# Performance work log

Hardware: AMD Instinct MI355X
Metric: run time of the kernel (lower is better)

The kernel has to match this reference:

```python
import jax, jax.numpy as jnp
import numpy as np

B, H, W, C = 16, 32, 32, 512
HEADS, DHEAD = 8, 64  # head * channel == C
GROUPS, EPS = 32, 1e-5


def setup_inputs() -> dict:
    key = jax.random.key(0)
    ks = jax.random.split(key, 6)
    return {
        "x": jax.random.normal(ks[0], (B, H, W, C), jnp.float32),
        "gn_gamma": jnp.ones((C,), jnp.float32),
        "gn_beta": jnp.zeros((C,), jnp.float32),
        "wq": jax.random.normal(ks[1], (C, HEADS * DHEAD), jnp.float32) * 0.02,
        "wk": jax.random.normal(ks[2], (C, HEADS * DHEAD), jnp.float32) * 0.02,
        "wv": jax.random.normal(ks[3], (C, HEADS * DHEAD), jnp.float32) * 0.02,
        "conv_w": jax.random.normal(ks[4], (3, 3, HEADS * DHEAD, C), jnp.float32) * 0.02,
        "conv_b": jnp.zeros((C,), jnp.float32),
    }


def _group_norm(x, gamma, beta):
    b, h, w, c = x.shape
    xg = x.reshape(b, h, w, GROUPS, c // GROUPS)
    mean = jnp.mean(xg, axis=(1, 2, 4), keepdims=True)
    var = jnp.var(xg, axis=(1, 2, 4), keepdims=True)
    xn = (xg - mean) * jax.lax.rsqrt(var + EPS)
    return xn.reshape(b, h, w, c) * gamma + beta


def reference(x, gn_gamma, gn_beta, wq, wk, wv, conv_w, conv_b):
    xn = _group_norm(x, gn_gamma, gn_beta)          # [B,H,W,C]
    t = xn.reshape(B, H * W, C)                      # tokens [B,S,C]
    q = (t @ wq).reshape(B, H * W, HEADS, DHEAD)
    k = (t @ wk).reshape(B, H * W, HEADS, DHEAD)
    v = (t @ wv).reshape(B, H * W, HEADS, DHEAD)
    scale = 1.0 / jnp.sqrt(jnp.asarray(DHEAD, q.dtype))
    scores = jnp.einsum("bqhd,bkhd->bhqk", q, k) * scale  # [B,HEADS,S,S]
    weights = jax.nn.softmax(scores, axis=-1)
    out = jnp.einsum("bhqk,bkhd->bqhd", weights, v)       # [B,S,HEADS,DHEAD]
    out = out.reshape(B, H, W, HEADS * DHEAD)
    y = jax.lax.conv_general_dilated(
        out, conv_w, window_strides=(1, 1), padding=((1, 1), (1, 1)),
        dimension_numbers=("NHWC", "HWIO", "NHWC")) + conv_b
    return y + x
```

## Files before the change

kernel.cpp:

```cpp
#include <hip/hip_runtime.h>
#include <hip/hip_bf16.h>

#define Bn 16
#define Cc 512
#define Ss 1024
#define HEADS 8
#define DHEAD 64
#define GROUPS 32
#define CPG 16
#define EPSv 1e-5f
#define Mtok (Bn*Ss)
#define QKVS 1536
#define PROW 34
#define PIMG (PROW*PROW)

typedef __hip_bfloat16 bf16;
typedef __attribute__((ext_vector_type(8))) short short8;
typedef __attribute__((ext_vector_type(4))) float f32x4;

union U4 { uint4 u; bf16 h[8]; };
union B4 { ushort4 u; bf16 h[4]; };

__device__ __forceinline__ void stage16(const bf16* g, bf16* l) {
    __builtin_amdgcn_global_load_lds((const __attribute__((address_space(1))) void*)g,
                                     (__attribute__((address_space(3))) void*)l,
                                     16, 0, 0);
}

__global__ __launch_bounds__(256) void wtrans(const float* __restrict__ src,
                                              bf16* __restrict__ dst) {
    size_t off = (size_t)blockIdx.y * 262144;
    int t = blockIdx.x * 256 + threadIdx.x;
    int n = t & 511, k8 = (t >> 9) * 8;
    const float* s = src + off + (size_t)k8 * 512 + n;
    U4 o;
#pragma unroll
    for (int j = 0; j < 8; j++) o.h[j] = __float2bfloat16(s[(size_t)j * 512]);
    *(uint4*)(dst + off + (size_t)n * 512 + k8) = o.u;
}

__global__ __launch_bounds__(256) void gn_stats(const float* __restrict__ x,
                                                float* __restrict__ stats) {
    int bg = blockIdx.x;
    int b = bg >> 5, g = bg & 31;
    int tid = threadIdx.x;
    const size_t base = (size_t)b * Ss * Cc + g * CPG;
    float sum = 0.f, sq = 0.f;
    for (int i = tid; i < 4096; i += 256) {
        int s = i >> 2, c4 = (i & 3) * 4;
        float4 t = *(const float4*)(x + base + (size_t)s * Cc + c4);
        sum += t.x + t.y + t.z + t.w;
        sq  += t.x * t.x + t.y * t.y + t.z * t.z + t.w * t.w;
    }
    __shared__ float s1[4], s2[4];
#pragma unroll
    for (int off = 32; off > 0; off >>= 1) {
        sum += __shfl_down(sum, off);
        sq  += __shfl_down(sq,  off);
    }
    if ((tid & 63) == 0) { s1[tid >> 6] = sum; s2[tid >> 6] = sq; }
    __syncthreads();
    if (tid == 0) {
        float S = s1[0] + s1[1] + s1[2] + s1[3];
        float Q = s2[0] + s2[1] + s2[2] + s2[3];
        float mean = S * (1.f / 16384.f);
        float var  = Q * (1.f / 16384.f) - mean * mean;
        stats[bg * 2 + 0] = mean;
        stats[bg * 2 + 1] = rsqrtf(var + EPSv);
    }
}

__global__ __launch_bounds__(256) void gn_apply(const float* __restrict__ x,
                                                const float* __restrict__ stats,
                                                const float* __restrict__ gamma,
                                                const float* __restrict__ beta,
                                                bf16* __restrict__ xn) {
    size_t i = (size_t)blockIdx.x * 256 + threadIdx.x;
    size_t e = i * 4;
    int c0 = (int)(e & (Cc - 1));
    int token = (int)(e >> 9);
    int b = token >> 10;
    int g = c0 >> 4;
    float mean = stats[(b * 32 + g) * 2 + 0];
    float rstd = stats[(b * 32 + g) * 2 + 1];
    float4 t  = *(const float4*)(x + e);
    float4 gm = *(const float4*)(gamma + c0);
    float4 bt = *(const float4*)(beta + c0);
    B4 o;
    o.h[0] = __float2bfloat16((t.x - mean) * rstd * gm.x + bt.x);
    o.h[1] = __float2bfloat16((t.y - mean) * rstd * gm.y + bt.y);
    o.h[2] = __float2bfloat16((t.z - mean) * rstd * gm.z + bt.z);
    o.h[3] = __float2bfloat16((t.w - mean) * rstd * gm.w + bt.w);
    *(ushort4*)(xn + e) = o.u;
}

__global__ __launch_bounds__(256) void zero_pad(bf16* __restrict__ Pad) {
    int idx = blockIdx.x * 256 + threadIdx.x;
    int b = idx / (132 * 64);
    int rem = idx - b * 132 * 64;
    int t = rem >> 6, seg = rem & 63;
    int r, c;
    if (t < 34)      { r = 0;  c = t; }
    else if (t < 68) { r = 33; c = t - 34; }
    else { int u = t - 68; r = 1 + (u >> 1); c = (u & 1) * 33; }
    uint4 z = {0u, 0u, 0u, 0u};
    *(uint4*)(Pad + ((size_t)b * PIMG + r * PROW + c) * Cc + seg * 8) = z;
}

__global__ __launch_bounds__(256) void gemm_qkv(const bf16* __restrict__ A,
                                                const bf16* __restrict__ Wt,
                                                bf16* __restrict__ C) {
    __shared__ __align__(16) bf16 As[128][32];
    __shared__ __align__(16) bf16 Bs[128][32];
    int tid = threadIdx.x;
    int wave = tid >> 6, lane = tid & 63;
    int l15 = lane & 15, quad = lane >> 4;
    int wm = wave >> 1, wn = wave & 1;
    int m0 = blockIdx.y * 128, n0 = blockIdx.x * 128;
    int lr = lane >> 2, kseg = (lane & 3) * 8;
    int ar0 = wave * 32 + lr;

    const bf16* ga = A  + (size_t)(m0 + ar0) * Cc + kseg;
    const bf16* gb = Wt + (size_t)(n0 + ar0) * Cc + kseg;
    bf16* la0 = &As[wave * 32][0];
    bf16* la1 = &As[wave * 32 + 16][0];
    bf16* lb0 = &Bs[wave * 32][0];
    bf16* lb1 = &Bs[wave * 32 + 16][0];

    f32x4 acc[4][4] = {};
    for (int k0 = 0; k0 < 512; k0 += 32) {
        __syncthreads();
        stage16(ga + k0,                  la0);
        stage16(ga + k0 + (size_t)16 * Cc, la1);
        stage16(gb + k0,                  lb0);
        stage16(gb + k0 + (size_t)16 * Cc, lb1);
        __syncthreads();
        short8 af[4], bfv[4];
#pragma unroll
        for (int mt = 0; mt < 4; mt++) af[mt]  = *(const short8*)&As[wm * 64 + mt * 16 + l15][quad * 8];
#pragma unroll
        for (int nt = 0; nt < 4; nt++) bfv[nt] = *(const short8*)&Bs[wn * 64 + nt * 16 + l15][quad * 8];
#pragma unroll
        for (int mt = 0; mt < 4; mt++)
#pragma unroll
            for (int nt = 0; nt < 4; nt++)
                acc[mt][nt] = __builtin_amdgcn_mfma_f32_16x16x32_bf16(af[mt], bfv[nt], acc[mt][nt], 0, 0, 0);
    }
#pragma unroll
    for (int mt = 0; mt < 4; mt++)
#pragma unroll
        for (int r = 0; r < 4; r++) {
            size_t row = (size_t)(m0 + wm * 64 + mt * 16 + quad * 4 + r) * QKVS + n0 + wn * 64 + l15;
#pragma unroll
            for (int nt = 0; nt < 4; nt++)
                C[row + nt * 16] = __float2bfloat16(acc[mt][nt][r]);
        }
}

__global__ __launch_bounds__(256) void attention_mfma(const bf16* __restrict__ QKV,
                                                      bf16* __restrict__ Pad) {
    int blk = blockIdx.x;
    int qt = blk & 15;
    int bh = blk >> 4;
    int h = bh & (HEADS - 1), b = bh >> 3;
    int tid = threadIdx.x;
    int wave = tid >> 6, lane = tid & 63;
    int l15 = lane & 15, quad = lane >> 4;

    __shared__ __align__(16) bf16 Ks[2][32][72];
    __shared__ __align__(16) bf16 Vt[2][64][40];
    __shared__ __align__(16) bf16 Ps[4][16][40];

    const size_t base = (size_t)b * Ss * QKVS + h * DHEAD;
    const bf16* kbase = QKV + base + 512;
    const bf16* vbase = QKV + base + 1024;

    int q0 = qt * 64 + wave * 16;
    const bf16* qrow = QKV + base + (size_t)(q0 + l15) * QKVS + quad * 8;
    short8 qf0 = *(const short8*)(qrow);
    short8 qf1 = *(const short8*)(qrow + 32);

    f32x4 oacc[4] = {{0.f,0.f,0.f,0.f},{0.f,0.f,0.f,0.f},{0.f,0.f,0.f,0.f},{0.f,0.f,0.f,0.f}};
    float lsum[4] = {0.f, 0.f, 0.f, 0.f};
    const f32x4 zero4 = {0.f, 0.f, 0.f, 0.f};

    int tok = tid & 31, d0 = (tid >> 5) * 8;

    uint4 nk, nv;
    {
        const size_t rb = (size_t)tok * QKVS + d0;
        nk = *(const uint4*)(kbase + rb);
        nv = *(const uint4*)(vbase + rb);
    }
    *(uint4*)&Ks[0][tok][d0] = nk;
    { U4 u; u.u = nv;
#pragma unroll
      for (int i = 0; i < 8; i++) Vt[0][d0 + i][tok] = u.h[i]; }
    __syncthreads();

    for (int c = 0; c < 32; ++c) {
        int buf = c & 1;
        if (c + 1 < 32) {
            const size_t rb = (size_t)((c + 1) * 32 + tok) * QKVS + d0;
            nk = *(const uint4*)(kbase + rb);
            nv = *(const uint4*)(vbase + rb);
        }
#pragma unroll
        for (int kg = 0; kg < 2; kg++) {
            short8 kf0 = *(const short8*)&Ks[buf][kg * 16 + l15][quad * 8];
            short8 kf1 = *(const short8*)&Ks[buf][kg * 16 + l15][32 + quad * 8];
            f32x4 s = __builtin_amdgcn_mfma_f32_16x16x32_bf16(qf0, kf0, zero4, 0, 0, 0);
            s = __builtin_amdgcn_mfma_f32_16x16x32_bf16(qf1, kf1, s, 0, 0, 0);
#pragma unroll
            for (int r = 0; r < 4; r++) {
                float p = __expf(s[r] * 0.125f);
                lsum[r] += p;
                Ps[wave][quad * 4 + r][kg * 16 + l15] = __float2bfloat16(p);
            }
        }
        short8 pf = *(const short8*)&Ps[wave][l15][quad * 8];
#pragma unroll
        for (int dt = 0; dt < 4; dt++) {
            short8 vf = *(const short8*)&Vt[buf][dt * 16 + l15][quad * 8];
            oacc[dt] = __builtin_amdgcn_mfma_f32_16x16x32_bf16(pf, vf, oacc[dt], 0, 0, 0);
        }
        if (c + 1 < 32) {
            *(uint4*)&Ks[buf ^ 1][tok][d0] = nk;
            U4 u; u.u = nv;
#pragma unroll
            for (int i = 0; i < 8; i++) Vt[buf ^ 1][d0 + i][tok] = u.h[i];
        }
        __syncthreads();
    }

#pragma unroll
    for (int r = 0; r < 4; r++) {
#pragma unroll
        for (int m = 1; m < 16; m <<= 1) lsum[r] += __shfl_xor(lsum[r], m);
    }
#pragma unroll
    for (int r = 0; r < 4; r++) {
        float inv = 1.f / lsum[r];
        int s = q0 + quad * 4 + r;
        size_t rowoff = ((size_t)(b * PROW + (s >> 5) + 1) * PROW + (s & 31) + 1) * Cc + h * DHEAD;
#pragma unroll
        for (int dt = 0; dt < 4; dt++)
            Pad[rowoff + dt * 16 + l15] = __float2bfloat16(oacc[dt][r] * inv);
    }
}

__global__ __launch_bounds__(256) void conv_mfma(const bf16* __restrict__ Pad,
                                                 const bf16* __restrict__ Wct,
                                                 const float* __restrict__ bias,
                                                 const float* __restrict__ xres,
                                                 float* __restrict__ out) {
    __shared__ __align__(16) bf16 As[136 * 32];
    __shared__ __align__(16) bf16 Bs[3][128][32];

    int tid = threadIdx.x;
    int wave = tid >> 6, lane = tid & 63;
    int l15 = lane & 15, quad = lane >> 4;
    int wm = wave >> 1, wn = wave & 1;
    int m0 = blockIdx.y * 128, n0 = blockIdx.x * 128;

    int b = m0 >> 10, oh0 = (m0 & 1023) >> 5;

    int lr = lane >> 2, kseg = (lane & 3) * 8;
    const bf16* gwp = Wct + (size_t)(n0 + wave * 32 + lr) * Cc + kseg;

    int t1 = tid >> 2,          r1 = t1 / 34, col1 = t1 - r1 * 34;
    int t2 = (tid + 256) >> 2,  r2 = t2 / 34, col2 = t2 - r2 * 34;
    int t3 = (tid + 512) >> 2,  r3 = t3 / 34, col3 = t3 - r3 * 34;
    int ks = (tid & 3) * 8;
    const size_t dyStride = (size_t)PROW * Cc;
    size_t pa1 = ((size_t)b * PIMG + (size_t)(oh0 + r1) * PROW + col1) * Cc + ks;
    size_t pa2 = ((size_t)b * PIMG + (size_t)(oh0 + r2) * PROW + col2) * Cc + ks;
    size_t pa3 = ((size_t)b * PIMG + (size_t)(oh0 + r3) * PROW + col3) * Cc + ks;
    bf16* aB0 = As + wave * 512;
    bf16* aB1 = As + 2048 + wave * 512;
    bf16* aB2 = As + 4096;

    int arow[4];
#pragma unroll
    for (int mt = 0; mt < 4; mt++)
        arow[mt] = (wm * 2 + (mt >> 1)) * 34 + (mt & 1) * 16 + l15;

    f32x4 acc[4][4] = {};
    for (int dyi = 0; dyi < 3; ++dyi) {
        const bf16* gA = Pad + (size_t)dyi * dyStride;
        const bf16* gW = gwp + (size_t)(dyi * 3) * (Cc * Cc);
        for (int k0 = 0; k0 < 512; k0 += 32) {
            __syncthreads();
            stage16(gA + pa1 + k0, aB0);
            stage16(gA + pa2 + k0, aB1);
            if (tid < 32) stage16(gA + pa3 + k0, aB2);
#pragma unroll
            for (int t = 0; t < 3; t++) {
                const bf16* gwt = gW + (size_t)t * (Cc * Cc) + k0;
                stage16(gwt,                   &Bs[t][wave * 32][0]);
                stage16(gwt + (size_t)16 * Cc, &Bs[t][wave * 32 + 16][0]);
            }
            __syncthreads();
#pragma unroll
            for (int dxi = 0; dxi < 3; dxi++) {
                short8 af[4], bfv[4];
#pragma unroll
                for (int mt = 0; mt < 4; mt++)
                    af[mt] = *(const short8*)&As[(arow[mt] + dxi) * 32 + quad * 8];
#pragma unroll
                for (int nt = 0; nt < 4; nt++)
                    bfv[nt] = *(const short8*)&Bs[dxi][wn * 64 + nt * 16 + l15][quad * 8];
#pragma unroll
                for (int mt = 0; mt < 4; mt++)
#pragma unroll
                    for (int nt = 0; nt < 4; nt++)
                        acc[mt][nt] = __builtin_amdgcn_mfma_f32_16x16x32_bf16(af[mt], bfv[nt], acc[mt][nt], 0, 0, 0);
            }
        }
    }
#pragma unroll
    for (int mt = 0; mt < 4; mt++)
#pragma unroll
        for (int r = 0; r < 4; r++) {
            size_t row = (size_t)(m0 + wm * 64 + mt * 16 + quad * 4 + r) * Cc + n0 + wn * 64 + l15;
#pragma unroll
            for (int nt = 0; nt < 4; nt++) {
                int n = n0 + wn * 64 + nt * 16 + l15;
                out[row + nt * 16] = acc[mt][nt][r] + bias[n] + xres[row + nt * 16];
            }
        }
}

extern "C" void kernel_launch(void* const* d_in, const int* in_sizes, int n_in,
                              void* d_out, int out_size, void* d_ws, size_t ws_size,
                              hipStream_t stream) {
    const float* x     = (const float*)d_in[0];
    const float* gamma = (const float*)d_in[1];
    const float* beta  = (const float*)d_in[2];
    const float* wq    = (const float*)d_in[3];
    const float* wk    = (const float*)d_in[4];
    const float* wv    = (const float*)d_in[5];
    const float* convw = (const float*)d_in[6];
    const float* convb = (const float*)d_in[7];
    float* out = (float*)d_out;

    char* ws = (char*)d_ws;
    bf16*  pad   = (bf16*)ws;
    float* stats = (float*)ws;
    bf16*  xn    = (bf16*)(ws + 4096);
    bf16*  wt    = (bf16*)(ws + 4096 + ((size_t)16 << 20));
    bf16*  qkv   = (bf16*)(ws + ((size_t)19 << 20));
    bf16*  wct   = (bf16*)(ws + ((size_t)67 << 20));

    wtrans<<<dim3(128, 1), 256, 0, stream>>>(wq, wt);
    wtrans<<<dim3(128, 1), 256, 0, stream>>>(wk, wt + 262144);
    wtrans<<<dim3(128, 1), 256, 0, stream>>>(wv, wt + 524288);
    wtrans<<<dim3(128, 9), 256, 0, stream>>>(convw, wct);

    gn_stats<<<dim3(Bn * GROUPS), 256, 0, stream>>>(x, stats);
    gn_apply<<<dim3(Mtok * Cc / (4 * 256)), 256, 0, stream>>>(x, stats, gamma, beta, xn);

    gemm_qkv<<<dim3(QKVS / 128, Mtok / 128), 256, 0, stream>>>(xn, wt, qkv);

    zero_pad<<<dim3(528), 256, 0, stream>>>(pad);
    attention_mfma<<<dim3(Bn * HEADS * (Ss / 64)), 256, 0, stream>>>(qkv, pad);

    conv_mfma<<<dim3(Cc / 128, Mtok / 128), 256, 0, stream>>>(pad, wct, convb, x, out);
}
```

Before: 345.0 us.

## Double-buffer conv LDS tiles to overlap global prefetch with MFMA

The 3x3 conv kernel's nested dy/k loops are flattened into one loop of 48 steps. The A and B tiles are now double-buffered in LDS, so the async global-to-LDS loads for the next step are issued before computing the current one, with explicit vmcnt waits and barriers. The fragments for all three dx taps are loaded up front, and launch bounds now ask for 2 blocks per CU. This is meant to hide global load latency behind the MFMA work, at the cost of twice the LDS footprint and more registers for the fragments.

```diff
diff --git a/kernel.cpp b/kernel.cpp
--- a/kernel.cpp
+++ b/kernel.cpp
@@ -249,20 +249,19 @@
     }
 }
 
-__global__ __launch_bounds__(256) void conv_mfma(const bf16* __restrict__ Pad,
-                                                 const bf16* __restrict__ Wct,
-                                                 const float* __restrict__ bias,
-                                                 const float* __restrict__ xres,
-                                                 float* __restrict__ out) {
-    __shared__ __align__(16) bf16 As[136 * 32];
-    __shared__ __align__(16) bf16 Bs[3][128][32];
+__global__ __launch_bounds__(256, 2) void conv_mfma(const bf16* __restrict__ Pad,
+                                                    const bf16* __restrict__ Wct,
+                                                    const float* __restrict__ bias,
+                                                    const float* __restrict__ xres,
+                                                    float* __restrict__ out) {
+    __shared__ __align__(16) bf16 As[2][136 * 32];
+    __shared__ __align__(16) bf16 Bs[2][3][128][32];
 
     int tid = threadIdx.x;
     int wave = tid >> 6, lane = tid & 63;
     int l15 = lane & 15, quad = lane >> 4;
     int wm = wave >> 1, wn = wave & 1;
     int m0 = blockIdx.y * 128, n0 = blockIdx.x * 128;
-
     int b = m0 >> 10, oh0 = (m0 & 1023) >> 5;
 
     int lr = lane >> 2, kseg = (lane & 3) * 8;
@@ -273,51 +272,66 @@
     int t3 = (tid + 512) >> 2,  r3 = t3 / 34, col3 = t3 - r3 * 34;
     int ks = (tid & 3) * 8;
     const size_t dyStride = (size_t)PROW * Cc;
-    size_t pa1 = ((size_t)b * PIMG + (size_t)(oh0 + r1) * PROW + col1) * Cc + ks;
-    size_t pa2 = ((size_t)b * PIMG + (size_t)(oh0 + r2) * PROW + col2) * Cc + ks;
-    size_t pa3 = ((size_t)b * PIMG + (size_t)(oh0 + r3) * PROW + col3) * Cc + ks;
-    bf16* aB0 = As + wave * 512;
-    bf16* aB1 = As + 2048 + wave * 512;
-    bf16* aB2 = As + 4096;
+    const bf16* pA1 = Pad + ((size_t)b * PIMG + (size_t)(oh0 + r1) * PROW + col1) * Cc + ks;
+    const bf16* pA2 = Pad + ((size_t)b * PIMG + (size_t)(oh0 + r2) * PROW + col2) * Cc + ks;
+    const bf16* pA3 = Pad + ((size_t)b * PIMG + (size_t)(oh0 + r3) * PROW + col3) * Cc + ks;
 
     int arow[4];
 #pragma unroll
     for (int mt = 0; mt < 4; mt++)
         arow[mt] = (wm * 2 + (mt >> 1)) * 34 + (mt & 1) * 16 + l15;
 
+    auto stage_it = [&](int it, int p) {
+        int dyi = it >> 4;
+        int k0 = (it & 15) << 5;
+        size_t aoff = (size_t)dyi * dyStride + k0;
+        stage16(pA1 + aoff, &As[p][wave * 512]);
+        stage16(pA2 + aoff, &As[p][2048 + wave * 512]);
+        if (tid < 32) stage16(pA3 + aoff, &As[p][4096]);
+        const bf16* gW = gwp + (size_t)(dyi * 3) * (Cc * Cc) + k0;
+#pragma unroll
+        for (int t = 0; t < 3; t++) {
+            const bf16* gwt = gW + (size_t)t * (Cc * Cc);
+            stage16(gwt,                   &Bs[p][t][wave * 32][0]);
+            stage16(gwt + (size_t)16 * Cc, &Bs[p][t][wave * 32 + 16][0]);
+        }
+    };
+
     f32x4 acc[4][4] = {};
-    for (int dyi = 0; dyi < 3; ++dyi) {
-        const bf16* gA = Pad + (size_t)dyi * dyStride;
-        const bf16* gW = gwp + (size_t)(dyi * 3) * (Cc * Cc);
-        for (int k0 = 0; k0 < 512; k0 += 32) {
-            __syncthreads();
-            stage16(gA + pa1 + k0, aB0);
-            stage16(gA + pa2 + k0, aB1);
-            if (tid < 32) stage16(gA + pa3 + k0, aB2);
-#pragma unroll
-            for (int t = 0; t < 3; t++) {
-                const bf16* gwt = gW + (size_t)t * (Cc * Cc) + k0;
-                stage16(gwt,                   &Bs[t][wave * 32][0]);
-                stage16(gwt + (size_t)16 * Cc, &Bs[t][wave * 32 + 16][0]);
-            }
-            __syncthreads();
-#pragma unroll
-            for (int dxi = 0; dxi < 3; dxi++) {
-                short8 af[4], bfv[4];
-#pragma unroll
-                for (int mt = 0; mt < 4; mt++)
-                    af[mt] = *(const short8*)&As[(arow[mt] + dxi) * 32 + quad * 8];
+    stage_it(0, 0);
+    for (int it = 0; it < 48; ++it) {
+        int p = it & 1;
+        if (it + 1 < 48) {
+            stage_it(it + 1, p ^ 1);
+            asm volatile("s_waitcnt vmcnt(8)" ::: "memory");
+        } else {
+            asm volatile("s_waitcnt vmcnt(0)" ::: "memory");
+        }
+        __builtin_amdgcn_s_barrier();
+
+        short8 af[3][4], bfv[3][4];
+#pragma unroll
+        for (int dxi = 0; dxi < 3; dxi++) {
+#pragma unroll
+            for (int mt = 0; mt < 4; mt++)
+                af[dxi][mt] = *(const short8*)&As[p][(arow[mt] + dxi) * 32 + quad * 8];
+#pragma unroll
+            for (int nt = 0; nt < 4; nt++)
+                bfv[dxi][nt] = *(const short8*)&Bs[p][dxi][wn * 64 + nt * 16 + l15][quad * 8];
+        }
+        asm volatile("s_waitcnt lgkmcnt(0)" ::: "memory");
+        __builtin_amdgcn_sched_barrier(0);
+        __builtin_amdgcn_s_barrier();
+
+#pragma unroll
+        for (int dxi = 0; dxi < 3; dxi++)
+#pragma unroll
+            for (int mt = 0; mt < 4; mt++)
 #pragma unroll
                 for (int nt = 0; nt < 4; nt++)
-                    bfv[nt] = *(const short8*)&Bs[dxi][wn * 64 + nt * 16 + l15][quad * 8];
-#pragma unroll
-                for (int mt = 0; mt < 4; mt++)
-#pragma unroll
-                    for (int nt = 0; nt < 4; nt++)
-                        acc[mt][nt] = __builtin_amdgcn_mfma_f32_16x16x32_bf16(af[mt], bfv[nt], acc[mt][nt], 0, 0, 0);
-            }
-        }
-    }
+                    acc[mt][nt] = __builtin_amdgcn_mfma_f32_16x16x32_bf16(af[dxi][mt], bfv[dxi][nt], acc[mt][nt], 0, 0, 0);
+    }
+
 #pragma unroll
     for (int mt = 0; mt < 4; mt++)
 #pragma unroll
```

Measured after the change: 321.5 us. 1.07x faster.
